# Kernel optimization log

Measured on AMD Instinct MI355X. Metric: run time of the kernel, lower is better.

## Reference

```python
import jax, jax.numpy as jnp
import numpy as np

B, N, F_IN, F_OUT = 4, 4096, 64, 64
ALPHA = 0.2  # LeakyReLU negative slope
NEG_INF = -9e15


def setup_inputs() -> dict:
    key = jax.random.key(0)
    k1, k2, k3, k4 = jax.random.split(key, 4)
    h = jax.random.normal(k1, (B, N, F_IN), dtype=jnp.float32)
    adj = jax.random.randint(k2, (B, N, N), 0, 2, dtype=jnp.int32)
    # xavier_uniform-like init (gain 1.414)
    lim_w = 1.414 * np.sqrt(6.0 / (F_IN + F_OUT))
    W = jax.random.uniform(k3, (F_IN, F_OUT), dtype=jnp.float32, minval=-lim_w, maxval=lim_w)
    lim_a = 1.414 * np.sqrt(6.0 / (2 * F_OUT + 1))
    a = jax.random.uniform(k4, (2 * F_OUT, 1), dtype=jnp.float32, minval=-lim_a, maxval=lim_a)
    return {"h": h, "adj": adj, "W": W, "a": a}


def reference(h, adj, W, a):
    # Wh: [B, N, F_out]
    Wh = jnp.matmul(h, W)
    a1 = a[:F_OUT, 0]   # [F_out]
    a2 = a[F_OUT:, 0]   # [F_out]
    # e[b,i,j] = LeakyReLU(Wh[b,i].a1 + Wh[b,j].a2)  (decomposed, avoids O(N^2*2F) concat)
    ei = jnp.einsum('bnf,f->bn', Wh, a1)  # source term
    ej = jnp.einsum('bnf,f->bn', Wh, a2)  # target term
    e = ei[:, :, None] + ej[:, None, :]   # [B, N, N]
    e = jnp.where(e > 0, e, ALPHA * e)    # LeakyReLU
    att = jnp.where(adj > 0, e, NEG_INF)
    att = jax.nn.softmax(att, axis=-1)
    h_prime = jnp.matmul(att, Wh)         # [B, N, F_out]
    return jax.nn.elu(h_prime)
```

## Files before the change

### kernel.cpp

```cpp
#include <hip/hip_runtime.h>
#include <stdint.h>

#define N_NODES 4096
#define F_DIM   64
#define LRELU_ALPHA 0.2f

typedef _Float16 f16;
typedef __attribute__((ext_vector_type(8))) _Float16 half8;
typedef __attribute__((ext_vector_type(4))) float f32x4;

__global__ __launch_bounds__(256) void gat_pp(
    const float* __restrict__ h, const float* __restrict__ W,
    const float* __restrict__ a, const int* __restrict__ adj,
    float* __restrict__ ei, float* __restrict__ ej,
    f16* __restrict__ whB, float* __restrict__ blockmax,
    uint32_t* __restrict__ bits)
{
  __shared__ float sh_h[4][F_DIM];
  __shared__ f16 tile[F_DIM][16];
  __shared__ float wmax[4];
  const int t = threadIdx.x, w = t >> 6, lane = t & 63;
  const int bid = blockIdx.x;
  const int pid = bid / 17;

  if (bid % 17 != 0) {
    const int r = bid - 1 - pid;
    const int* row = adj + (size_t)r * N_NODES;
    const int jw0 = w * 1024;

    int v[16];
#pragma unroll
    for (int p = 0; p < 16; ++p)
      v[p] = row[jw0 + p * 64 + lane];

#pragma unroll
    for (int p = 0; p < 16; ++p) {
      const unsigned long long m = __ballot(v[p] > 0);
      if (lane == 0)
        *(uint64_t*)(bits + (size_t)r * 128 + ((jw0 + p * 64) >> 5)) = m;
    }
    return;
  }

  const int n0 = pid * 16;
  const int b  = n0 >> 12;
  const int nl0 = n0 & (N_NODES - 1);

  float wcol[F_DIM];
#pragma unroll
  for (int k = 0; k < F_DIM; ++k) wcol[k] = W[k * F_DIM + lane];
  const float a1 = a[lane], a2 = a[F_DIM + lane];

  float runmax = -3e38f;
  for (int r = 0; r < 4; ++r) {
    const int loc = w * 4 + r;
    const int n = n0 + loc;
    const float hv = h[(size_t)n * F_DIM + lane];
    sh_h[w][lane] = hv;
    float wh = 0.f;
#pragma unroll
    for (int k = 0; k < F_DIM; k += 4) {
      const float4 hb = *(const float4*)(&sh_h[w][k]);
      wh = fmaf(hb.x, wcol[k + 0], wh);
      wh = fmaf(hb.y, wcol[k + 1], wh);
      wh = fmaf(hb.z, wcol[k + 2], wh);
      wh = fmaf(hb.w, wcol[k + 3], wh);
    }
    float s1 = wh * a1, s2 = wh * a2;
#pragma unroll
    for (int off = 32; off; off >>= 1) {
      s1 += __shfl_xor(s1, off);
      s2 += __shfl_xor(s2, off);
    }
    if (lane == 0) { ei[n] = s1; ej[n] = s2; }
    runmax = fmaxf(runmax, s2);
    tile[lane][loc] = (f16)wh;
  }
  if (lane == 0) wmax[w] = runmax;
  __syncthreads();

  {
    const int jc = nl0 >> 5;
    const int q0 = (nl0 >> 3) & 3;
    const int fc = t >> 6;
    const int r6 = t & 63;
    const int qp = r6 >> 5;
    const int m  = (r6 >> 1) & 15;
    const int xh = (t & 1) * 4;
    const int loc = qp * 8 + xh;
    f16* dst = whB + (((size_t)(b * 128 + jc)) * 4 + fc) * 512
                   + ((q0 + qp) * 16 + m) * 8 + xh;
    *(uint2*)dst = *(const uint2*)(&tile[fc * 16 + m][loc]);
  }
  if (t == 0)
    blockmax[pid] =
        fmaxf(fmaxf(wmax[0], wmax[1]), fmaxf(wmax[2], wmax[3]));
}

__global__ __launch_bounds__(512, 4) void gat_attn(
    const uint32_t* __restrict__ bits, const float* __restrict__ ei,
    const float* __restrict__ ej, const f16* __restrict__ whB,
    const float* __restrict__ blockmax, float* __restrict__ out)
{
  __shared__ float num_lds[8][32][F_DIM];
  __shared__ float den_lds[8][32];

  const int t = threadIdx.x, w = t >> 6, lane = t & 63;
  const int quad = lane >> 4, m = lane & 15;
  const int b  = blockIdx.x >> 7;
  const int i0 = (blockIdx.x & 127) * 32;
  const int rowg0 = b * N_NODES + i0 + m;
  const int rowg1 = rowg0 + 16;

  float maxej;
  {
    const float4 v = *(const float4*)(blockmax + b * 256 + lane * 4);
    maxej = fmaxf(fmaxf(v.x, v.y), fmaxf(v.z, v.w));
#pragma unroll
    for (int off = 32; off; off >>= 1)
      maxej = fmaxf(maxej, __shfl_xor(maxej, off));
  }

  const float ei0 = ei[rowg0], ei1 = ei[rowg1];
  float bnd0 = ei0 + maxej;
  bnd0 = fmaxf(bnd0, LRELU_ALPHA * bnd0);
  float bnd1 = ei1 + maxej;
  bnd1 = fmaxf(bnd1, LRELU_ALPHA * bnd1);
  const float c10 = ei0 - bnd0, c20 = LRELU_ALPHA * ei0 - bnd0;
  const float c11 = ei1 - bnd1, c21 = LRELU_ALPHA * ei1 - bnd1;

  const float* ejb = ej + b * N_NODES;
  const uint32_t* bitrow0 = bits + (size_t)rowg0 * 128 + w * 16;
  const uint32_t* bitrow1 = bits + (size_t)rowg1 * 128 + w * 16;
  const f16* whw = whB + ((size_t)(b * 128 + w * 16)) * 2048 + lane * 8;

  f32x4 acc0[4] = {{0.f,0.f,0.f,0.f},{0.f,0.f,0.f,0.f},
                   {0.f,0.f,0.f,0.f},{0.f,0.f,0.f,0.f}};
  f32x4 acc1[4] = {{0.f,0.f,0.f,0.f},{0.f,0.f,0.f,0.f},
                   {0.f,0.f,0.f,0.f},{0.f,0.f,0.f,0.f}};
  float den0 = 0.f, den1 = 0.f;
  const int jbase = w * (N_NODES / 8);

  for (int jo = 0; jo < 4; ++jo) {
    const uint4 dq0 = *(const uint4*)(bitrow0 + jo * 4);
    const uint4 dq1 = *(const uint4*)(bitrow1 + jo * 4);
    const uint32_t dws0[4] = {dq0.x, dq0.y, dq0.z, dq0.w};
    const uint32_t dws1[4] = {dq1.x, dq1.y, dq1.z, dq1.w};

#pragma unroll
    for (int ji = 0; ji < 4; ++ji) {
      const int jc = jo * 4 + ji;
      const int jk = jbase + jc * 32 + quad * 8;
      const uint32_t dw0 = dws0[ji], dw1 = dws1[ji];

      float ejA[8];
      *(float4*)(&ejA[0]) = *(const float4*)(ejb + jk);
      *(float4*)(&ejA[4]) = *(const float4*)(ejb + jk + 4);

      const f16* wjc = whw + (size_t)jc * 2048;
      half8 bf[4];
#pragma unroll
      for (int fc = 0; fc < 4; ++fc)
        bf[fc] = *(const half8*)(wjc + fc * 512);

      half8 pa0, pa1;
#pragma unroll
      for (int x = 0; x < 8; ++x) {
        const float e = ejA[x];
        const float g0 = fmaxf(e + c10, fmaf(LRELU_ALPHA, e, c20));
        const float g1 = fmaxf(e + c11, fmaf(LRELU_ALPHA, e, c21));
        const float p0 = ((dw0 >> (quad * 8 + x)) & 1u) ? __expf(g0) : 0.f;
        const float p1 = ((dw1 >> (quad * 8 + x)) & 1u) ? __expf(g1) : 0.f;
        pa0[x] = (f16)p0;
        pa1[x] = (f16)p1;
        den0 += (float)pa0[x];
        den1 += (float)pa1[x];
      }

#pragma unroll
      for (int fc = 0; fc < 4; ++fc) {
        acc0[fc] = __builtin_amdgcn_mfma_f32_16x16x32_f16(pa0, bf[fc], acc0[fc], 0, 0, 0);
        acc1[fc] = __builtin_amdgcn_mfma_f32_16x16x32_f16(pa1, bf[fc], acc1[fc], 0, 0, 0);
      }
    }
  }

  den0 += __shfl_xor(den0, 16);
  den0 += __shfl_xor(den0, 32);
  den1 += __shfl_xor(den1, 16);
  den1 += __shfl_xor(den1, 32);
  if (lane < 16) {
    den_lds[w][lane] = den0;
    den_lds[w][lane + 16] = den1;
  }

#pragma unroll
  for (int fc = 0; fc < 4; ++fc)
#pragma unroll
    for (int rg = 0; rg < 4; ++rg) {
      num_lds[w][quad * 4 + rg][fc * 16 + m] = acc0[fc][rg];
      num_lds[w][16 + quad * 4 + rg][fc * 16 + m] = acc1[fc][rg];
    }
  __syncthreads();

#pragma unroll
  for (int k = 0; k < 4; ++k) {
    const int idx = k * 512 + t;
    const int il = idx >> 6, f = idx & 63;
    float num = 0.f, d = 0.f;
#pragma unroll
    for (int ww = 0; ww < 8; ++ww) {
      num += num_lds[ww][il][f];
      d   += den_lds[ww][il];
    }
    float v = (d > 0.f) ? (num / d) : 0.f;
    v = (v > 0.f) ? v : expm1f(v);
    out[((size_t)(b * N_NODES + i0 + il)) * F_DIM + f] = v;
  }
}

extern "C" void kernel_launch(void* const* d_in, const int* in_sizes, int n_in,
                              void* d_out, int out_size, void* d_ws, size_t ws_size,
                              hipStream_t stream) {
  const float* h   = (const float*)d_in[0];
  const int*   adj = (const int*)d_in[1];
  const float* W   = (const float*)d_in[2];
  const float* a   = (const float*)d_in[3];
  float* out = (float*)d_out;

  char* ws = (char*)d_ws;
  float*    ei       = (float*)ws;
  float*    ej       = (float*)(ws + 65536);
  float*    blockmax = (float*)(ws + 131072);
  f16*      whB      = (f16*)(ws + 135168);
  uint32_t* bits     = (uint32_t*)(ws + 2232320);

  hipLaunchKernelGGL(gat_pp, dim3(17408), dim3(256), 0, stream,
                     h, W, a, adj, ei, ej, whB, blockmax, bits);
  hipLaunchKernelGGL(gat_attn, dim3(512), dim3(512), 0, stream,
                     bits, ei, ej, whB, blockmax, out);
}
```

Measured before the change: 393.9 us.

## Pack adjacency bitmask with one row per wave and simplify attention loop

The bitmask pass now gives each wave a whole adjacency row, looping over four batches of 16 coalesced loads, so the grid shrinks from 17408 to 5120 blocks, with one Wh block interleaved per four bitmask blocks. This cuts block-scheduling overhead in the dominant 268MB adjacency read while keeping many loads in flight. The attention kernel flattens its loop into a non-unrolled 16-iteration loop with per-iteration bit loads. It also accumulates the denominator in fp32 using two split partial sums instead of rounding through fp16, which slightly changes numerics.

After: 392.6 us. About the same (-0.3%).

```diff
diff --git a/kernel.cpp b/kernel.cpp
--- a/kernel.cpp
+++ b/kernel.cpp
@@ -21,23 +21,25 @@
   __shared__ float wmax[4];
   const int t = threadIdx.x, w = t >> 6, lane = t & 63;
   const int bid = blockIdx.x;
-  const int pid = bid / 17;
-
-  if (bid % 17 != 0) {
-    const int r = bid - 1 - pid;
-    const int* row = adj + (size_t)r * N_NODES;
-    const int jw0 = w * 1024;
-
-    int v[16];
-#pragma unroll
-    for (int p = 0; p < 16; ++p)
-      v[p] = row[jw0 + p * 64 + lane];
-
-#pragma unroll
-    for (int p = 0; p < 16; ++p) {
-      const unsigned long long m = __ballot(v[p] > 0);
-      if (lane == 0)
-        *(uint64_t*)(bits + (size_t)r * 128 + ((jw0 + p * 64) >> 5)) = m;
+  const int pid = bid / 5;
+
+  if (bid % 5 != 0) {
+    const int pk = bid - 1 - pid;
+    const int row = pk * 4 + w;
+    const int* rowp = adj + (size_t)row * N_NODES + lane;
+    uint64_t* dst = (uint64_t*)(bits + (size_t)row * 128);
+
+#pragma unroll 1
+    for (int bch = 0; bch < 4; ++bch) {
+      int v[16];
+#pragma unroll
+      for (int s = 0; s < 16; ++s)
+        v[s] = rowp[(bch * 16 + s) * 64];
+#pragma unroll
+      for (int s = 0; s < 16; ++s) {
+        const unsigned long long m = __ballot(v[s] > 0);
+        if (lane == 0) dst[bch * 16 + s] = m;
+      }
     }
     return;
   }
@@ -107,6 +109,7 @@
 
   const int t = threadIdx.x, w = t >> 6, lane = t & 63;
   const int quad = lane >> 4, m = lane & 15;
+  const int kq = quad * 8;
   const int b  = blockIdx.x >> 7;
   const int i0 = (blockIdx.x & 127) * 32;
   const int rowg0 = b * N_NODES + i0 + m;
@@ -129,7 +132,7 @@
   const float c10 = ei0 - bnd0, c20 = LRELU_ALPHA * ei0 - bnd0;
   const float c11 = ei1 - bnd1, c21 = LRELU_ALPHA * ei1 - bnd1;
 
-  const float* ejb = ej + b * N_NODES;
+  const float* ejb = ej + b * N_NODES + w * 512;
   const uint32_t* bitrow0 = bits + (size_t)rowg0 * 128 + w * 16;
   const uint32_t* bitrow1 = bits + (size_t)rowg1 * 128 + w * 16;
   const f16* whw = whB + ((size_t)(b * 128 + w * 16)) * 2048 + lane * 8;
@@ -138,53 +141,45 @@
                    {0.f,0.f,0.f,0.f},{0.f,0.f,0.f,0.f}};
   f32x4 acc1[4] = {{0.f,0.f,0.f,0.f},{0.f,0.f,0.f,0.f},
                    {0.f,0.f,0.f,0.f},{0.f,0.f,0.f,0.f}};
-  float den0 = 0.f, den1 = 0.f;
-  const int jbase = w * (N_NODES / 8);
-
-  for (int jo = 0; jo < 4; ++jo) {
-    const uint4 dq0 = *(const uint4*)(bitrow0 + jo * 4);
-    const uint4 dq1 = *(const uint4*)(bitrow1 + jo * 4);
-    const uint32_t dws0[4] = {dq0.x, dq0.y, dq0.z, dq0.w};
-    const uint32_t dws1[4] = {dq1.x, dq1.y, dq1.z, dq1.w};
-
-#pragma unroll
-    for (int ji = 0; ji < 4; ++ji) {
-      const int jc = jo * 4 + ji;
-      const int jk = jbase + jc * 32 + quad * 8;
-      const uint32_t dw0 = dws0[ji], dw1 = dws1[ji];
-
-      float ejA[8];
-      *(float4*)(&ejA[0]) = *(const float4*)(ejb + jk);
-      *(float4*)(&ejA[4]) = *(const float4*)(ejb + jk + 4);
-
-      const f16* wjc = whw + (size_t)jc * 2048;
-      half8 bf[4];
-#pragma unroll
-      for (int fc = 0; fc < 4; ++fc)
-        bf[fc] = *(const half8*)(wjc + fc * 512);
-
-      half8 pa0, pa1;
-#pragma unroll
-      for (int x = 0; x < 8; ++x) {
-        const float e = ejA[x];
-        const float g0 = fmaxf(e + c10, fmaf(LRELU_ALPHA, e, c20));
-        const float g1 = fmaxf(e + c11, fmaf(LRELU_ALPHA, e, c21));
-        const float p0 = ((dw0 >> (quad * 8 + x)) & 1u) ? __expf(g0) : 0.f;
-        const float p1 = ((dw1 >> (quad * 8 + x)) & 1u) ? __expf(g1) : 0.f;
-        pa0[x] = (f16)p0;
-        pa1[x] = (f16)p1;
-        den0 += (float)pa0[x];
-        den1 += (float)pa1[x];
-      }
-
-#pragma unroll
-      for (int fc = 0; fc < 4; ++fc) {
-        acc0[fc] = __builtin_amdgcn_mfma_f32_16x16x32_f16(pa0, bf[fc], acc0[fc], 0, 0, 0);
-        acc1[fc] = __builtin_amdgcn_mfma_f32_16x16x32_f16(pa1, bf[fc], acc1[fc], 0, 0, 0);
-      }
-    }
-  }
-
+  float dA0 = 0.f, dB0 = 0.f, dA1 = 0.f, dB1 = 0.f;
+
+#pragma unroll 1
+  for (int jc = 0; jc < 16; ++jc) {
+    const uint32_t dw0 = bitrow0[jc];
+    const uint32_t dw1 = bitrow1[jc];
+
+    float ejA[8];
+    *(float4*)(&ejA[0]) = *(const float4*)(ejb + jc * 32 + kq);
+    *(float4*)(&ejA[4]) = *(const float4*)(ejb + jc * 32 + kq + 4);
+
+    const f16* wjc = whw + (size_t)jc * 2048;
+    half8 bf[4];
+#pragma unroll
+    for (int fc = 0; fc < 4; ++fc)
+      bf[fc] = *(const half8*)(wjc + fc * 512);
+
+    half8 pa0, pa1;
+#pragma unroll
+    for (int x = 0; x < 8; ++x) {
+      const float e = ejA[x];
+      const float g0 = fmaxf(e + c10, fmaf(LRELU_ALPHA, e, c20));
+      const float g1 = fmaxf(e + c11, fmaf(LRELU_ALPHA, e, c21));
+      const float p0 = ((dw0 >> (kq + x)) & 1u) ? __expf(g0) : 0.f;
+      const float p1 = ((dw1 >> (kq + x)) & 1u) ? __expf(g1) : 0.f;
+      pa0[x] = (f16)p0;
+      pa1[x] = (f16)p1;
+      if (x & 1) { dB0 += p0; dB1 += p1; }
+      else       { dA0 += p0; dA1 += p1; }
+    }
+
+#pragma unroll
+    for (int fc = 0; fc < 4; ++fc) {
+      acc0[fc] = __builtin_amdgcn_mfma_f32_16x16x32_f16(pa0, bf[fc], acc0[fc], 0, 0, 0);
+      acc1[fc] = __builtin_amdgcn_mfma_f32_16x16x32_f16(pa1, bf[fc], acc1[fc], 0, 0, 0);
+    }
+  }
+
+  float den0 = dA0 + dB0, den1 = dA1 + dB1;
   den0 += __shfl_xor(den0, 16);
   den0 += __shfl_xor(den0, 32);
   den1 += __shfl_xor(den1, 16);
@@ -235,7 +230,7 @@
   f16*      whB      = (f16*)(ws + 135168);
   uint32_t* bits     = (uint32_t*)(ws + 2232320);
 
-  hipLaunchKernelGGL(gat_pp, dim3(17408), dim3(256), 0, stream,
+  hipLaunchKernelGGL(gat_pp, dim3(5120), dim3(256), 0, stream,
                      h, W, a, adj, ei, ej, whB, blockmax, bits);
   hipLaunchKernelGGL(gat_attn, dim3(512), dim3(512), 0, stream,
                      bits, ei, ej, whB, blockmax, out);
```
